# Kernel optimization log

Measured on AMD Instinct MI355X. Metric: run time of the kernel, lower is better.

## Reference

```python
import jax, jax.numpy as jnp
import numpy as np
from jax import lax

EPS = 1e-6


def setup_inputs() -> dict:
    key = jax.random.key(0)
    k1, k2, k3, k4 = jax.random.split(key, 4)
    B, M, N = 256, 256, 256
    A_re = jax.random.normal(k1, (B, M, N), dtype=jnp.float32)
    A_im = jax.random.normal(k2, (B, M, N), dtype=jnp.float32)
    v_re = jax.random.uniform(k3, (B, N, 1), dtype=jnp.float32)
    v_im = jax.random.uniform(k4, (B, N, 1), dtype=jnp.float32)
    return {"A_re": A_re, "A_im": A_im, "v_re": v_re, "v_im": v_im, "num_iter": 30}


def reference(A_re, A_im, v_re, v_im, num_iter):
    A = (A_re + 1j * A_im).astype(jnp.complex64)          # [B, M, N]
    v = (v_re + 1j * v_im).astype(jnp.complex64)          # [B, N, 1]
    # AhA = A^H A : [B, N, N]
    AhA = jnp.einsum('bmn,bmk->bnk', jnp.conj(A), A)

    def step(v, _):
        v = jnp.matmul(AhA, v)                            # [B, N, 1]
        # ||v||_2 over the N axis -> [B, 1]
        eig = jnp.sqrt(jnp.sum(v.real**2 + v.imag**2, axis=1))
        v = v / (eig[:, :, None] + EPS)
        return v, eig

    v, eigs = lax.scan(step, v, None, length=num_iter)
    return eigs[-1].reshape(-1)                           # [B]
```

## Files before the change

### kernel.cpp

```cpp
#include <hip/hip_runtime.h>
#include <cstdint>

typedef _Float16 f16;
typedef _Float16 f16x2 __attribute__((ext_vector_type(2)));
typedef _Float16 f16x8 __attribute__((ext_vector_type(8)));
typedef float    f32x4 __attribute__((ext_vector_type(4)));

static __device__ __forceinline__ uint32_t pack2(float x, float y) {
    f16 hx = (f16)x, hy = (f16)y;
    uint32_t ux = __builtin_bit_cast(unsigned short, hx);
    uint32_t uy = __builtin_bit_cast(unsigned short, hy);
    return ux | (uy << 16);
}

__global__ __launch_bounds__(512, 2) void k_gemm(const float* __restrict__ Are,
                                                 const float* __restrict__ Aim,
                                                 f16* __restrict__ AhAre,
                                                 f16* __restrict__ AhAim) {
    const int tid = threadIdx.x;
    const int b = blockIdx.x;

    __shared__ __align__(16) f16 ls[2][256 * 32];

    const int l = tid & 63, g = tid >> 6;
    const int lr = l & 15, lk = l >> 4;

    const int u = tid & 15;
    const int fp = tid >> 4;
    const int su = u >> 2, uq = u & 3;

    f32x4 cR[16], cI[16], dR[8], dI[8];
#pragma unroll
    for (int j = 0; j < 16; ++j) { cR[j] = (f32x4)0.0f; cI[j] = (f32x4)0.0f; }
#pragma unroll
    for (int j = 0; j < 8; ++j)  { dR[j] = (f32x4)0.0f; dI[j] = (f32x4)0.0f; }

    for (int m0 = 0; m0 < 256; m0 += 32) {
        __syncthreads();
        float4 v[2][4];
#pragma unroll
        for (int t = 0; t < 2; ++t) {
            const float* sp = (t ? Aim : Are) + (size_t)b * 65536
                            + (size_t)(m0 + 2 * u) * 256 + fp * 8;
            v[t][0] = *(const float4*)(sp);
            v[t][1] = *(const float4*)(sp + 4);
            v[t][2] = *(const float4*)(sp + 256);
            v[t][3] = *(const float4*)(sp + 260);
        }
#pragma unroll
        for (int t = 0; t < 2; ++t) {
            float xv[8] = {v[t][0].x, v[t][0].y, v[t][0].z, v[t][0].w,
                           v[t][1].x, v[t][1].y, v[t][1].z, v[t][1].w};
            float yv[8] = {v[t][2].x, v[t][2].y, v[t][2].z, v[t][2].w,
                           v[t][3].x, v[t][3].y, v[t][3].z, v[t][3].w};
            uint32_t* lw = (uint32_t*)&ls[t][0];
#pragma unroll
            for (int i = 0; i < 8; ++i) {
                int r = fp * 8 + i;
                int s = su ^ ((r >> 1) & 3);
                lw[r * 16 + s * 4 + uq] = pack2(xv[i], yv[i]);
            }
        }
        __syncthreads();

        const int r1 = 16 * g + lr;
        const int r2 = 128 + 16 * g + lr;
        const int s1 = lk ^ ((r1 >> 1) & 3);
        const int s2 = lk ^ ((r2 >> 1) & 3);
        f16x8 a1re = *(const f16x8*)(&ls[0][r1 * 32 + s1 * 8]);
        uint4 u1   = *(const uint4*)(&ls[1][r1 * 32 + s1 * 8]);
        f16x8 a2re = *(const f16x8*)(&ls[0][r2 * 32 + s2 * 8]);
        uint4 u2   = *(const uint4*)(&ls[1][r2 * 32 + s2 * 8]);
        f16x8 a1im = __builtin_bit_cast(f16x8, u1);
        f16x8 a2im = __builtin_bit_cast(f16x8, u2);
        uint4 n1 = make_uint4(u1.x ^ 0x80008000u, u1.y ^ 0x80008000u,
                              u1.z ^ 0x80008000u, u1.w ^ 0x80008000u);
        uint4 n2 = make_uint4(u2.x ^ 0x80008000u, u2.y ^ 0x80008000u,
                              u2.z ^ 0x80008000u, u2.w ^ 0x80008000u);
        f16x8 na1 = __builtin_bit_cast(f16x8, n1);
        f16x8 na2 = __builtin_bit_cast(f16x8, n2);

#pragma unroll
        for (int j = 0; j < 16; ++j) {
            int rb = 16 * j + lr;
            int sb = lk ^ ((rb >> 1) & 3);
            f16x8 bre = *(const f16x8*)(&ls[0][rb * 32 + sb * 8]);
            f16x8 bim = *(const f16x8*)(&ls[1][rb * 32 + sb * 8]);
            cR[j] = __builtin_amdgcn_mfma_f32_16x16x32_f16(a1re, bre, cR[j], 0, 0, 0);
            cR[j] = __builtin_amdgcn_mfma_f32_16x16x32_f16(a1im, bim, cR[j], 0, 0, 0);
            cI[j] = __builtin_amdgcn_mfma_f32_16x16x32_f16(a1re, bim, cI[j], 0, 0, 0);
            cI[j] = __builtin_amdgcn_mfma_f32_16x16x32_f16(na1,  bre, cI[j], 0, 0, 0);
            if (j >= 8) {
                dR[j-8] = __builtin_amdgcn_mfma_f32_16x16x32_f16(a2re, bre, dR[j-8], 0, 0, 0);
                dR[j-8] = __builtin_amdgcn_mfma_f32_16x16x32_f16(a2im, bim, dR[j-8], 0, 0, 0);
                dI[j-8] = __builtin_amdgcn_mfma_f32_16x16x32_f16(a2re, bim, dI[j-8], 0, 0, 0);
                dI[j-8] = __builtin_amdgcn_mfma_f32_16x16x32_f16(na2,  bre, dI[j-8], 0, 0, 0);
            }
        }
    }

    f16* oR = AhAre + (size_t)b * 65536;
    f16* oI = AhAim + (size_t)b * 65536;

#pragma unroll
    for (int j = 0; j < 16; ++j)
#pragma unroll
        for (int r = 0; r < 4; ++r) {
            int n = 16 * g + lk * 4 + r;
            int c = 16 * j + lr;
            oR[(size_t)n * 256 + c] = (f16)cR[j][r];
            oI[(size_t)n * 256 + c] = (f16)cI[j][r];
        }
#pragma unroll
    for (int j = 0; j < 8; ++j)
#pragma unroll
        for (int r = 0; r < 4; ++r) {
            int n = 128 + 16 * g + lk * 4 + r;
            int c = 128 + 16 * j + lr;
            oR[(size_t)n * 256 + c] = (f16)dR[j][r];
            oI[(size_t)n * 256 + c] = (f16)dI[j][r];
        }

    f16* lsm = &ls[0][0];
    const int jj_out = tid >> 2, qtr = tid & 3;

    __syncthreads();
#pragma unroll
    for (int j = 8; j < 16; ++j)
#pragma unroll
        for (int r = 0; r < 4; ++r) {
            int jj = 16 * (j - 8) + lr;
            int nn = 16 * g + lk * 4 + r;
            lsm[jj * 128 + nn] = (f16)cR[j][r];
        }
    __syncthreads();
    {
        const f16* srow = lsm + jj_out * 128 + qtr * 32;
        f16* drow = oR + (size_t)(128 + jj_out) * 256 + qtr * 32;
#pragma unroll
        for (int ch = 0; ch < 4; ++ch)
            *(uint4*)(void*)(drow + ch * 8) = *(const uint4*)(srow + ch * 8);
    }
    __syncthreads();
#pragma unroll
    for (int j = 8; j < 16; ++j)
#pragma unroll
        for (int r = 0; r < 4; ++r) {
            int jj = 16 * (j - 8) + lr;
            int nn = 16 * g + lk * 4 + r;
            lsm[jj * 128 + nn] = (f16)(-cI[j][r]);
        }
    __syncthreads();
    {
        const f16* srow = lsm + jj_out * 128 + qtr * 32;
        f16* drow = oI + (size_t)(128 + jj_out) * 256 + qtr * 32;
#pragma unroll
        for (int ch = 0; ch < 4; ++ch)
            *(uint4*)(void*)(drow + ch * 8) = *(const uint4*)(srow + ch * 8);
    }
}

static __device__ __forceinline__ void matvec2(const f16x8 (&afr)[2][16],
                                               const f16* __restrict__ vs, int h,
                                               float4 (&y)[2]) {
    f16x8 bf[16];
#pragma unroll
    for (int c = 0; c < 16; ++c) bf[c] = *(const f16x8*)(vs + 32 * c + 8 * h);
    f32x4 P0[2], P1[2];
#pragma unroll
    for (int rg = 0; rg < 2; ++rg) { P0[rg] = (f32x4)0.0f; P1[rg] = (f32x4)0.0f; }
#pragma unroll
    for (int c = 0; c < 16; ++c) {
#pragma unroll
        for (int rg = 0; rg < 2; ++rg) {
            if (c & 1) P1[rg] = __builtin_amdgcn_mfma_f32_16x16x32_f16(afr[rg][c], bf[c], P1[rg], 0, 0, 0);
            else       P0[rg] = __builtin_amdgcn_mfma_f32_16x16x32_f16(afr[rg][c], bf[c], P0[rg], 0, 0, 0);
        }
    }
#pragma unroll
    for (int rg = 0; rg < 2; ++rg)
        y[rg] = make_float4(P0[rg][0] + P1[rg][0], P0[rg][1] + P1[rg][1],
                            P0[rg][2] + P1[rg][2], P0[rg][3] + P1[rg][3]);
}

__global__ __launch_bounds__(512, 2) void k_power(const f16* __restrict__ AhAre,
                                                  const f16* __restrict__ AhAim,
                                                  const float* __restrict__ vre,
                                                  const float* __restrict__ vim,
                                                  const int* __restrict__ pniter,
                                                  float* __restrict__ out) {
    const int tid = threadIdx.x;
    const int b = blockIdx.x;
    const int l = tid & 63;
    const int g = tid >> 6;
    const int sel = l & 15;
    const int h = l >> 4;

    __shared__ __align__(16) f16 v0h[2][512];
    __shared__ __align__(16) f16 v1h[2][512];
    __shared__ __align__(16) float part[2][8];

    f16x8 afr[2][16];
#pragma unroll
    for (int rg = 0; rg < 2; ++rg) {
        const int m = 32 * g + 16 * rg + sel;
        const f16* bR = AhAre + (size_t)b * 65536 + (size_t)m * 256 + 8 * h;
        const f16* bI = AhAim + (size_t)b * 65536 + (size_t)m * 256 + 8 * h;
#pragma unroll
        for (int c = 0; c < 8; ++c) {
            afr[rg][c]     = *(const f16x8*)(bR + 32 * c);
            afr[rg][8 + c] = *(const f16x8*)(bI + 32 * c);
        }
    }
#pragma unroll
    for (int rg = 0; rg < 2; ++rg)
#pragma unroll
        for (int c = 0; c < 16; ++c) asm volatile("" : "+a"(afr[rg][c]));

    if (tid < 256) {
        float xr = vre[b * 256 + tid], xi = vim[b * 256 + tid];
        v0h[0][tid]       = (f16)xr;
        v0h[0][256 + tid] = (f16)(-xi);
        v1h[0][tid]       = (f16)xi;
        v1h[0][256 + tid] = (f16)xr;
    }
    __syncthreads();

    const int niter = *pniter;
    const f16* vsel = (sel == 0) ? &v0h[0][0] : &v1h[0][0];

    float eig = 0.0f;

    auto npart = [&](int wb, const float4 (&y)[2]) {
        float s_ = 0.0f;
        if (sel < 2) {
#pragma unroll
            for (int rg = 0; rg < 2; ++rg)
                s_ += y[rg].x * y[rg].x + y[rg].y * y[rg].y
                    + y[rg].z * y[rg].z + y[rg].w * y[rg].w;
        }
        s_ += __shfl_xor(s_, 1, 64);
        s_ += __shfl_xor(s_, 16, 64);
        s_ += __shfl_xor(s_, 32, 64);
        if (l == 0) part[wb][g] = s_;
    };
    auto vwrite = [&](int wb, const float4 (&y)[2], float sc) {
        if (sel < 2) {
#pragma unroll
            for (int rg = 0; rg < 2; ++rg) {
                uint32_t w0 = pack2(y[rg].x * sc, y[rg].y * sc);
                uint32_t w1 = pack2(y[rg].z * sc, y[rg].w * sc);
                int m0 = 32 * g + 16 * rg + 4 * h;
                if (sel == 0) {
                    *(uint2*)(void*)(&v0h[wb][m0])       = make_uint2(w0, w1);
                    *(uint2*)(void*)(&v1h[wb][256 + m0]) = make_uint2(w0, w1);
                } else {
                    *(uint2*)(void*)(&v1h[wb][m0])       = make_uint2(w0, w1);
                    *(uint2*)(void*)(&v0h[wb][256 + m0]) =
                        make_uint2(w0 ^ 0x80008000u, w1 ^ 0x80008000u);
                }
            }
        }
    };
    auto psum = [&](int rb) -> float {
        float4 q0 = *(const float4*)(&part[rb][0]);
        float4 q1 = *(const float4*)(&part[rb][4]);
        return (q0.x + q0.y + q0.z + q0.w) + (q1.x + q1.y + q1.z + q1.w);
    };

    float sc_m1 = 1.0f;
    float nm2   = 1.0f;

    float4 y[2];

    if (niter >= 1) {
        matvec2(afr, vsel, h, y);
        npart(1, y);
        __syncthreads();
        float e1v = sqrtf(psum(1));
        float sc  = __builtin_amdgcn_rcpf(e1v + 1e-6f);
        vwrite(1, y, sc);
        eig = e1v;
        __syncthreads();
    }
    if (niter >= 2) {
        matvec2(afr, vsel + 512, h, y);
        npart(0, y);
        __syncthreads();
        float e2v = sqrtf(psum(0));
        float sc  = __builtin_amdgcn_rcpf(e2v + 1e-6f);
        vwrite(0, y, sc);
        eig = e2v;
        sc_m1 = sc;
        nm2   = 1.0f;
        __syncthreads();
    }

    int wr = 0;
    for (int t = 3; t <= niter; ++t) {
        const int rd = wr;
        wr ^= 1;
        float q   = psum(rd);
        float e1v = __builtin_amdgcn_sqrtf(q);
        float nm1 = e1v * sc_m1;
        float sc  = nm2 * __builtin_amdgcn_rcpf(e1v * nm1 + 1e-12f);
        matvec2(afr, vsel + (size_t)rd * 512, h, y);
        vwrite(wr, y, sc);
        npart(wr, y);
        nm2 = nm1; sc_m1 = sc;
        __syncthreads();
    }

    if (niter >= 3) {
        float qT = psum(wr);
        eig = sqrtf(qT) / (nm2 + 1e-12f);
    }
    if (tid == 0) out[b] = eig;
}

extern "C" void kernel_launch(void* const* d_in, const int* in_sizes, int n_in,
                              void* d_out, int out_size, void* d_ws, size_t ws_size,
                              hipStream_t stream) {
    const float* Are = (const float*)d_in[0];
    const float* Aim = (const float*)d_in[1];
    const float* vre = (const float*)d_in[2];
    const float* vim = (const float*)d_in[3];
    const int* niter = (const int*)d_in[4];
    float* out = (float*)d_out;

    f16* AhAre = (f16*)d_ws;
    f16* AhAim = (f16*)((char*)d_ws + (size_t)32 * 1024 * 1024);

    k_gemm<<<dim3(256), dim3(512), 0, stream>>>(Are, Aim, AhAre, AhAim);
    k_power<<<dim3(256), dim3(512), 0, stream>>>(AhAre, AhAim, vre, vim, niter, out);
}
```

Before: 97.59 us.

## Double-buffer LDS and prefetch next A tile during MFMA compute

Allocates two LDS buffers for the A^H A gemm and loads the next 32-row slab of A into registers while the current slab is being consumed by MFMAs. This removes one barrier per step and overlaps global load latency with compute. It doubles the LDS footprint and keeps prefetch registers live across the MFMA loop, which may raise register pressure.

Result: slower. 115.9 us (+18.7%).

```diff
diff --git a/kernel.cpp b/kernel.cpp
--- a/kernel.cpp
+++ b/kernel.cpp
@@ -20,7 +20,7 @@
     const int tid = threadIdx.x;
     const int b = blockIdx.x;
 
-    __shared__ __align__(16) f16 ls[2][256 * 32];
+    __shared__ __align__(16) f16 ls[2][2][256 * 32];
 
     const int l = tid & 63, g = tid >> 6;
     const int lr = l & 15, lk = l >> 4;
@@ -35,25 +35,28 @@
 #pragma unroll
     for (int j = 0; j < 8; ++j)  { dR[j] = (f32x4)0.0f; dI[j] = (f32x4)0.0f; }
 
-    for (int m0 = 0; m0 < 256; m0 += 32) {
-        __syncthreads();
-        float4 v[2][4];
-#pragma unroll
-        for (int t = 0; t < 2; ++t) {
-            const float* sp = (t ? Aim : Are) + (size_t)b * 65536
-                            + (size_t)(m0 + 2 * u) * 256 + fp * 8;
-            v[t][0] = *(const float4*)(sp);
-            v[t][1] = *(const float4*)(sp + 4);
-            v[t][2] = *(const float4*)(sp + 256);
-            v[t][3] = *(const float4*)(sp + 260);
-        }
+    float4 v[2][4];
+#pragma unroll
+    for (int t = 0; t < 2; ++t) {
+        const float* sp = (t ? Aim : Are) + (size_t)b * 65536
+                        + (size_t)(2 * u) * 256 + fp * 8;
+        v[t][0] = *(const float4*)(sp);
+        v[t][1] = *(const float4*)(sp + 4);
+        v[t][2] = *(const float4*)(sp + 256);
+        v[t][3] = *(const float4*)(sp + 260);
+    }
+
+#pragma unroll 2
+    for (int step = 0; step < 8; ++step) {
+        const int p = step & 1;
+
 #pragma unroll
         for (int t = 0; t < 2; ++t) {
             float xv[8] = {v[t][0].x, v[t][0].y, v[t][0].z, v[t][0].w,
                            v[t][1].x, v[t][1].y, v[t][1].z, v[t][1].w};
             float yv[8] = {v[t][2].x, v[t][2].y, v[t][2].z, v[t][2].w,
                            v[t][3].x, v[t][3].y, v[t][3].z, v[t][3].w};
-            uint32_t* lw = (uint32_t*)&ls[t][0];
+            uint32_t* lw = (uint32_t*)&ls[p][t][0];
 #pragma unroll
             for (int i = 0; i < 8; ++i) {
                 int r = fp * 8 + i;
@@ -61,16 +64,33 @@
                 lw[r * 16 + s * 4 + uq] = pack2(xv[i], yv[i]);
             }
         }
-        __syncthreads();
+
+        if (step < 7) {
+            const int m0n = 32 * (step + 1);
+#pragma unroll
+            for (int t = 0; t < 2; ++t) {
+                const float* sp = (t ? Aim : Are) + (size_t)b * 65536
+                                + (size_t)(m0n + 2 * u) * 256 + fp * 8;
+                v[t][0] = *(const float4*)(sp);
+                v[t][1] = *(const float4*)(sp + 4);
+                v[t][2] = *(const float4*)(sp + 256);
+                v[t][3] = *(const float4*)(sp + 260);
+            }
+        }
+
+        __syncthreads();
+
+        const f16* lsR = &ls[p][0][0];
+        const f16* lsI = &ls[p][1][0];
 
         const int r1 = 16 * g + lr;
         const int r2 = 128 + 16 * g + lr;
         const int s1 = lk ^ ((r1 >> 1) & 3);
         const int s2 = lk ^ ((r2 >> 1) & 3);
-        f16x8 a1re = *(const f16x8*)(&ls[0][r1 * 32 + s1 * 8]);
-        uint4 u1   = *(const uint4*)(&ls[1][r1 * 32 + s1 * 8]);
-        f16x8 a2re = *(const f16x8*)(&ls[0][r2 * 32 + s2 * 8]);
-        uint4 u2   = *(const uint4*)(&ls[1][r2 * 32 + s2 * 8]);
+        f16x8 a1re = *(const f16x8*)(&lsR[r1 * 32 + s1 * 8]);
+        uint4 u1   = *(const uint4*)(&lsI[r1 * 32 + s1 * 8]);
+        f16x8 a2re = *(const f16x8*)(&lsR[r2 * 32 + s2 * 8]);
+        uint4 u2   = *(const uint4*)(&lsI[r2 * 32 + s2 * 8]);
         f16x8 a1im = __builtin_bit_cast(f16x8, u1);
         f16x8 a2im = __builtin_bit_cast(f16x8, u2);
         uint4 n1 = make_uint4(u1.x ^ 0x80008000u, u1.y ^ 0x80008000u,
@@ -84,8 +104,8 @@
         for (int j = 0; j < 16; ++j) {
             int rb = 16 * j + lr;
             int sb = lk ^ ((rb >> 1) & 3);
-            f16x8 bre = *(const f16x8*)(&ls[0][rb * 32 + sb * 8]);
-            f16x8 bim = *(const f16x8*)(&ls[1][rb * 32 + sb * 8]);
+            f16x8 bre = *(const f16x8*)(&lsR[rb * 32 + sb * 8]);
+            f16x8 bim = *(const f16x8*)(&lsI[rb * 32 + sb * 8]);
             cR[j] = __builtin_amdgcn_mfma_f32_16x16x32_f16(a1re, bre, cR[j], 0, 0, 0);
             cR[j] = __builtin_amdgcn_mfma_f32_16x16x32_f16(a1im, bim, cR[j], 0, 0, 0);
             cI[j] = __builtin_amdgcn_mfma_f32_16x16x32_f16(a1re, bim, cI[j], 0, 0, 0);
@@ -121,7 +141,7 @@
             oI[(size_t)n * 256 + c] = (f16)dI[j][r];
         }
 
-    f16* lsm = &ls[0][0];
+    f16* lsm = &ls[0][0][0];
     const int jj_out = tid >> 2, qtr = tid & 3;
 
     __syncthreads();
```

## Split Hermitian Gram GEMM into three quadrant blocks per batch

Applied to the files above, without the earlier changes.

The A^H A kernel now launches three blocks per batch, each computing one 128x128 quadrant of the Hermitian result (top-left, top-right with mirrored lower-left, bottom-right), instead of one block computing the whole upper triangle. Each block holds half as many accumulators, so launch bounds rise to allow four blocks per CU. A remapping of the block index groups the three blocks of the same batch so they land on the same XCD and share A in cache. This adds parallelism and occupancy on 256 CUs, at the cost of re-reading A from memory or cache up to three times per batch.

Result: slower. 117.0 us (+19.9%).

```diff
diff --git a/kernel.cpp b/kernel.cpp
--- a/kernel.cpp
+++ b/kernel.cpp
@@ -2,7 +2,6 @@
 #include <cstdint>
 
 typedef _Float16 f16;
-typedef _Float16 f16x2 __attribute__((ext_vector_type(2)));
 typedef _Float16 f16x8 __attribute__((ext_vector_type(8)));
 typedef float    f32x4 __attribute__((ext_vector_type(4)));
 
@@ -13,76 +12,84 @@
     return ux | (uy << 16);
 }
 
-__global__ __launch_bounds__(512, 2) void k_gemm(const float* __restrict__ Are,
+__global__ __launch_bounds__(512, 4) void k_gemm(const float* __restrict__ Are,
                                                  const float* __restrict__ Aim,
                                                  f16* __restrict__ AhAre,
                                                  f16* __restrict__ AhAim) {
     const int tid = threadIdx.x;
-    const int b = blockIdx.x;
+    int bid0 = blockIdx.x;
+    int bid = (bid0 & 7) * 96 + (bid0 >> 3);
+    const int b  = bid / 3;
+    const int qq = bid - 3 * b;
+    const int R0 = (qq == 2) ? 128 : 0;
+    const int C0 = (qq == 0) ? 0 : 128;
+    const int nb0 = (qq == 2) ? 128 : 0;
+    const int boff = (qq == 1) ? 128 : 0;
 
     __shared__ __align__(16) f16 ls[2][256 * 32];
 
     const int l = tid & 63, g = tid >> 6;
     const int lr = l & 15, lk = l >> 4;
-
-    const int u = tid & 15;
-    const int fp = tid >> 4;
+    const int u = tid & 15, fp = tid >> 4;
     const int su = u >> 2, uq = u & 3;
 
-    f32x4 cR[16], cI[16], dR[8], dI[8];
-#pragma unroll
-    for (int j = 0; j < 16; ++j) { cR[j] = (f32x4)0.0f; cI[j] = (f32x4)0.0f; }
-#pragma unroll
-    for (int j = 0; j < 8; ++j)  { dR[j] = (f32x4)0.0f; dI[j] = (f32x4)0.0f; }
+    f16* oR = AhAre + (size_t)b * 65536;
+    f16* oI = AhAim + (size_t)b * 65536;
+
+    f32x4 cR[8], cI[8];
+#pragma unroll
+    for (int j = 0; j < 8; ++j) { cR[j] = (f32x4)0.0f; cI[j] = (f32x4)0.0f; }
 
     for (int m0 = 0; m0 < 256; m0 += 32) {
         __syncthreads();
-        float4 v[2][4];
 #pragma unroll
         for (int t = 0; t < 2; ++t) {
             const float* sp = (t ? Aim : Are) + (size_t)b * 65536
-                            + (size_t)(m0 + 2 * u) * 256 + fp * 8;
-            v[t][0] = *(const float4*)(sp);
-            v[t][1] = *(const float4*)(sp + 4);
-            v[t][2] = *(const float4*)(sp + 256);
-            v[t][3] = *(const float4*)(sp + 260);
-        }
-#pragma unroll
-        for (int t = 0; t < 2; ++t) {
-            float xv[8] = {v[t][0].x, v[t][0].y, v[t][0].z, v[t][0].w,
-                           v[t][1].x, v[t][1].y, v[t][1].z, v[t][1].w};
-            float yv[8] = {v[t][2].x, v[t][2].y, v[t][2].z, v[t][2].w,
-                           v[t][3].x, v[t][3].y, v[t][3].z, v[t][3].w};
+                            + (size_t)(m0 + 2 * u) * 256 + nb0 + fp * 4;
+            float4 x = *(const float4*)(sp);
+            float4 y = *(const float4*)(sp + 256);
+            float xv[4] = {x.x, x.y, x.z, x.w};
+            float yv[4] = {y.x, y.y, y.z, y.w};
             uint32_t* lw = (uint32_t*)&ls[t][0];
 #pragma unroll
-            for (int i = 0; i < 8; ++i) {
-                int r = fp * 8 + i;
+            for (int i = 0; i < 4; ++i) {
+                int r = fp * 4 + i;
                 int s = su ^ ((r >> 1) & 3);
                 lw[r * 16 + s * 4 + uq] = pack2(xv[i], yv[i]);
             }
         }
-        __syncthreads();
-
-        const int r1 = 16 * g + lr;
-        const int r2 = 128 + 16 * g + lr;
-        const int s1 = lk ^ ((r1 >> 1) & 3);
-        const int s2 = lk ^ ((r2 >> 1) & 3);
-        f16x8 a1re = *(const f16x8*)(&ls[0][r1 * 32 + s1 * 8]);
-        uint4 u1   = *(const uint4*)(&ls[1][r1 * 32 + s1 * 8]);
-        f16x8 a2re = *(const f16x8*)(&ls[0][r2 * 32 + s2 * 8]);
-        uint4 u2   = *(const uint4*)(&ls[1][r2 * 32 + s2 * 8]);
+        if (qq == 1) {
+#pragma unroll
+            for (int t = 0; t < 2; ++t) {
+                const float* sp = (t ? Aim : Are) + (size_t)b * 65536
+                                + (size_t)(m0 + 2 * u) * 256 + 128 + fp * 4;
+                float4 x = *(const float4*)(sp);
+                float4 y = *(const float4*)(sp + 256);
+                float xv[4] = {x.x, x.y, x.z, x.w};
+                float yv[4] = {y.x, y.y, y.z, y.w};
+                uint32_t* lw = (uint32_t*)&ls[t][0];
+#pragma unroll
+                for (int i = 0; i < 4; ++i) {
+                    int r = 128 + fp * 4 + i;
+                    int s = su ^ ((r >> 1) & 3);
+                    lw[r * 16 + s * 4 + uq] = pack2(xv[i], yv[i]);
+                }
+            }
+        }
+        __syncthreads();
+
+        const int ra = 16 * g + lr;
+        const int sa = lk ^ ((ra >> 1) & 3);
+        f16x8 a1re = *(const f16x8*)(&ls[0][ra * 32 + sa * 8]);
+        uint4 u1   = *(const uint4*)(&ls[1][ra * 32 + sa * 8]);
         f16x8 a1im = __builtin_bit_cast(f16x8, u1);
-        f16x8 a2im = __builtin_bit_cast(f16x8, u2);
         uint4 n1 = make_uint4(u1.x ^ 0x80008000u, u1.y ^ 0x80008000u,
                               u1.z ^ 0x80008000u, u1.w ^ 0x80008000u);
-        uint4 n2 = make_uint4(u2.x ^ 0x80008000u, u2.y ^ 0x80008000u,
-                              u2.z ^ 0x80008000u, u2.w ^ 0x80008000u);
         f16x8 na1 = __builtin_bit_cast(f16x8, n1);
-        f16x8 na2 = __builtin_bit_cast(f16x8, n2);
-
-#pragma unroll
-        for (int j = 0; j < 16; ++j) {
-            int rb = 16 * j + lr;
+
+#pragma unroll
+        for (int j = 0; j < 8; ++j) {
+            int rb = boff + 16 * j + lr;
             int sb = lk ^ ((rb >> 1) & 3);
             f16x8 bre = *(const f16x8*)(&ls[0][rb * 32 + sb * 8]);
             f16x8 bim = *(const f16x8*)(&ls[1][rb * 32 + sb * 8]);
@@ -90,73 +97,57 @@
             cR[j] = __builtin_amdgcn_mfma_f32_16x16x32_f16(a1im, bim, cR[j], 0, 0, 0);
             cI[j] = __builtin_amdgcn_mfma_f32_16x16x32_f16(a1re, bim, cI[j], 0, 0, 0);
             cI[j] = __builtin_amdgcn_mfma_f32_16x16x32_f16(na1,  bre, cI[j], 0, 0, 0);
-            if (j >= 8) {
-                dR[j-8] = __builtin_amdgcn_mfma_f32_16x16x32_f16(a2re, bre, dR[j-8], 0, 0, 0);
-                dR[j-8] = __builtin_amdgcn_mfma_f32_16x16x32_f16(a2im, bim, dR[j-8], 0, 0, 0);
-                dI[j-8] = __builtin_amdgcn_mfma_f32_16x16x32_f16(a2re, bim, dI[j-8], 0, 0, 0);
-                dI[j-8] = __builtin_amdgcn_mfma_f32_16x16x32_f16(na2,  bre, dI[j-8], 0, 0, 0);
-            }
-        }
-    }
-
-    f16* oR = AhAre + (size_t)b * 65536;
-    f16* oI = AhAim + (size_t)b * 65536;
-
-#pragma unroll
-    for (int j = 0; j < 16; ++j)
+        }
+    }
+
+#pragma unroll
+    for (int j = 0; j < 8; ++j)
 #pragma unroll
         for (int r = 0; r < 4; ++r) {
-            int n = 16 * g + lk * 4 + r;
-            int c = 16 * j + lr;
+            int n = R0 + 16 * g + lk * 4 + r;
+            int c = C0 + 16 * j + lr;
             oR[(size_t)n * 256 + c] = (f16)cR[j][r];
             oI[(size_t)n * 256 + c] = (f16)cI[j][r];
         }
-#pragma unroll
-    for (int j = 0; j < 8; ++j)
-#pragma unroll
-        for (int r = 0; r < 4; ++r) {
-            int n = 128 + 16 * g + lk * 4 + r;
-            int c = 128 + 16 * j + lr;
-            oR[(size_t)n * 256 + c] = (f16)dR[j][r];
-            oI[(size_t)n * 256 + c] = (f16)dI[j][r];
-        }
-
-    f16* lsm = &ls[0][0];
-    const int jj_out = tid >> 2, qtr = tid & 3;
-
-    __syncthreads();
-#pragma unroll
-    for (int j = 8; j < 16; ++j)
-#pragma unroll
-        for (int r = 0; r < 4; ++r) {
-            int jj = 16 * (j - 8) + lr;
-            int nn = 16 * g + lk * 4 + r;
-            lsm[jj * 128 + nn] = (f16)cR[j][r];
-        }
-    __syncthreads();
-    {
-        const f16* srow = lsm + jj_out * 128 + qtr * 32;
-        f16* drow = oR + (size_t)(128 + jj_out) * 256 + qtr * 32;
-#pragma unroll
-        for (int ch = 0; ch < 4; ++ch)
-            *(uint4*)(void*)(drow + ch * 8) = *(const uint4*)(srow + ch * 8);
-    }
-    __syncthreads();
-#pragma unroll
-    for (int j = 8; j < 16; ++j)
-#pragma unroll
-        for (int r = 0; r < 4; ++r) {
-            int jj = 16 * (j - 8) + lr;
-            int nn = 16 * g + lk * 4 + r;
-            lsm[jj * 128 + nn] = (f16)(-cI[j][r]);
-        }
-    __syncthreads();
-    {
-        const f16* srow = lsm + jj_out * 128 + qtr * 32;
-        f16* drow = oI + (size_t)(128 + jj_out) * 256 + qtr * 32;
-#pragma unroll
-        for (int ch = 0; ch < 4; ++ch)
-            *(uint4*)(void*)(drow + ch * 8) = *(const uint4*)(srow + ch * 8);
+
+    if (qq == 1) {
+        f16* lsm = &ls[0][0];
+        const int jjo = tid >> 2, qtr = tid & 3;
+
+        __syncthreads();
+#pragma unroll
+        for (int j = 0; j < 8; ++j)
+#pragma unroll
+            for (int r = 0; r < 4; ++r) {
+                int jj = 16 * j + lr;
+                int nn = 16 * g + lk * 4 + r;
+                lsm[jj * 128 + nn] = (f16)cR[j][r];
+            }
+        __syncthreads();
+        {
+            const f16* srow = lsm + jjo * 128 + qtr * 32;
+            f16* drow = oR + (size_t)(128 + jjo) * 256 + qtr * 32;
+#pragma unroll
+            for (int ch = 0; ch < 4; ++ch)
+                *(uint4*)(void*)(drow + ch * 8) = *(const uint4*)(srow + ch * 8);
+        }
+        __syncthreads();
+#pragma unroll
+        for (int j = 0; j < 8; ++j)
+#pragma unroll
+            for (int r = 0; r < 4; ++r) {
+                int jj = 16 * j + lr;
+                int nn = 16 * g + lk * 4 + r;
+                lsm[jj * 128 + nn] = (f16)(-cI[j][r]);
+            }
+        __syncthreads();
+        {
+            const f16* srow = lsm + jjo * 128 + qtr * 32;
+            f16* drow = oI + (size_t)(128 + jjo) * 256 + qtr * 32;
+#pragma unroll
+            for (int ch = 0; ch < 4; ++ch)
+                *(uint4*)(void*)(drow + ch * 8) = *(const uint4*)(srow + ch * 8);
+        }
     }
 }
 
@@ -331,6 +322,6 @@
     f16* AhAre = (f16*)d_ws;
     f16* AhAim = (f16*)((char*)d_ws + (size_t)32 * 1024 * 1024);
 
-    k_gemm<<<dim3(256), dim3(512), 0, stream>>>(Are, Aim, AhAre, AhAim);
+    k_gemm<<<dim3(768), dim3(512), 0, stream>>>(Are, Aim, AhAre, AhAim);
     k_power<<<dim3(256), dim3(512), 0, stream>>>(AhAre, AhAim, vre, vim, niter, out);
 }
```

## Split Hermitian GEMM into two phases with 64-deep K tiles and prefetch

Applied to the files above, without the earlier changes.

Restructures the A^H A kernel into two sequential phases: the first computes the top 128 rows (16 accumulator tiles), the second computes only the bottom-right block and loads just the right half of the columns. Each phase stages 64 rows of M per iteration and prefetches the next global tile into registers while the MFMAs run. Custom barriers with waitcnt and sched_barrier replace __syncthreads. This aims to shorten accumulator live ranges, hide global-load latency and halve barrier count, at the cost of doubled LDS footprint, which may reduce occupancy, and of re-reading A for the second phase.

After: 107.1 us. 9.8% more time.

```diff
diff --git a/kernel.cpp b/kernel.cpp
--- a/kernel.cpp
+++ b/kernel.cpp
@@ -2,7 +2,6 @@
 #include <cstdint>
 
 typedef _Float16 f16;
-typedef _Float16 f16x2 __attribute__((ext_vector_type(2)));
 typedef _Float16 f16x8 __attribute__((ext_vector_type(8)));
 typedef float    f32x4 __attribute__((ext_vector_type(4)));
 
@@ -11,6 +10,13 @@
     uint32_t ux = __builtin_bit_cast(unsigned short, hx);
     uint32_t uy = __builtin_bit_cast(unsigned short, hy);
     return ux | (uy << 16);
+}
+
+static __device__ __forceinline__ void lds_barrier() {
+    __builtin_amdgcn_sched_barrier(0);
+    asm volatile("s_waitcnt lgkmcnt(0)");
+    __builtin_amdgcn_s_barrier();
+    __builtin_amdgcn_sched_barrier(0);
 }
 
 __global__ __launch_bounds__(512, 2) void k_gemm(const float* __restrict__ Are,
@@ -20,143 +26,215 @@
     const int tid = threadIdx.x;
     const int b = blockIdx.x;
 
-    __shared__ __align__(16) f16 ls[2][256 * 32];
+    __shared__ __align__(16) f16 ls[2][256 * 64];
 
     const int l = tid & 63, g = tid >> 6;
     const int lr = l & 15, lk = l >> 4;
-
-    const int u = tid & 15;
-    const int fp = tid >> 4;
+    const int u = tid & 15, fp = tid >> 4;
     const int su = u >> 2, uq = u & 3;
-
-    f32x4 cR[16], cI[16], dR[8], dI[8];
-#pragma unroll
-    for (int j = 0; j < 16; ++j) { cR[j] = (f32x4)0.0f; cI[j] = (f32x4)0.0f; }
-#pragma unroll
-    for (int j = 0; j < 8; ++j)  { dR[j] = (f32x4)0.0f; dI[j] = (f32x4)0.0f; }
-
-    for (int m0 = 0; m0 < 256; m0 += 32) {
-        __syncthreads();
-        float4 v[2][4];
-#pragma unroll
-        for (int t = 0; t < 2; ++t) {
-            const float* sp = (t ? Aim : Are) + (size_t)b * 65536
-                            + (size_t)(m0 + 2 * u) * 256 + fp * 8;
-            v[t][0] = *(const float4*)(sp);
-            v[t][1] = *(const float4*)(sp + 4);
-            v[t][2] = *(const float4*)(sp + 256);
-            v[t][3] = *(const float4*)(sp + 260);
-        }
-#pragma unroll
-        for (int t = 0; t < 2; ++t) {
-            float xv[8] = {v[t][0].x, v[t][0].y, v[t][0].z, v[t][0].w,
-                           v[t][1].x, v[t][1].y, v[t][1].z, v[t][1].w};
-            float yv[8] = {v[t][2].x, v[t][2].y, v[t][2].z, v[t][2].w,
-                           v[t][3].x, v[t][3].y, v[t][3].z, v[t][3].w};
-            uint32_t* lw = (uint32_t*)&ls[t][0];
-#pragma unroll
-            for (int i = 0; i < 8; ++i) {
-                int r = fp * 8 + i;
-                int s = su ^ ((r >> 1) & 3);
-                lw[r * 16 + s * 4 + uq] = pack2(xv[i], yv[i]);
-            }
-        }
-        __syncthreads();
-
-        const int r1 = 16 * g + lr;
-        const int r2 = 128 + 16 * g + lr;
-        const int s1 = lk ^ ((r1 >> 1) & 3);
-        const int s2 = lk ^ ((r2 >> 1) & 3);
-        f16x8 a1re = *(const f16x8*)(&ls[0][r1 * 32 + s1 * 8]);
-        uint4 u1   = *(const uint4*)(&ls[1][r1 * 32 + s1 * 8]);
-        f16x8 a2re = *(const f16x8*)(&ls[0][r2 * 32 + s2 * 8]);
-        uint4 u2   = *(const uint4*)(&ls[1][r2 * 32 + s2 * 8]);
-        f16x8 a1im = __builtin_bit_cast(f16x8, u1);
-        f16x8 a2im = __builtin_bit_cast(f16x8, u2);
-        uint4 n1 = make_uint4(u1.x ^ 0x80008000u, u1.y ^ 0x80008000u,
-                              u1.z ^ 0x80008000u, u1.w ^ 0x80008000u);
-        uint4 n2 = make_uint4(u2.x ^ 0x80008000u, u2.y ^ 0x80008000u,
-                              u2.z ^ 0x80008000u, u2.w ^ 0x80008000u);
-        f16x8 na1 = __builtin_bit_cast(f16x8, n1);
-        f16x8 na2 = __builtin_bit_cast(f16x8, n2);
-
-#pragma unroll
-        for (int j = 0; j < 16; ++j) {
-            int rb = 16 * j + lr;
-            int sb = lk ^ ((rb >> 1) & 3);
-            f16x8 bre = *(const f16x8*)(&ls[0][rb * 32 + sb * 8]);
-            f16x8 bim = *(const f16x8*)(&ls[1][rb * 32 + sb * 8]);
-            cR[j] = __builtin_amdgcn_mfma_f32_16x16x32_f16(a1re, bre, cR[j], 0, 0, 0);
-            cR[j] = __builtin_amdgcn_mfma_f32_16x16x32_f16(a1im, bim, cR[j], 0, 0, 0);
-            cI[j] = __builtin_amdgcn_mfma_f32_16x16x32_f16(a1re, bim, cI[j], 0, 0, 0);
-            cI[j] = __builtin_amdgcn_mfma_f32_16x16x32_f16(na1,  bre, cI[j], 0, 0, 0);
-            if (j >= 8) {
-                dR[j-8] = __builtin_amdgcn_mfma_f32_16x16x32_f16(a2re, bre, dR[j-8], 0, 0, 0);
-                dR[j-8] = __builtin_amdgcn_mfma_f32_16x16x32_f16(a2im, bim, dR[j-8], 0, 0, 0);
-                dI[j-8] = __builtin_amdgcn_mfma_f32_16x16x32_f16(a2re, bim, dI[j-8], 0, 0, 0);
-                dI[j-8] = __builtin_amdgcn_mfma_f32_16x16x32_f16(na2,  bre, dI[j-8], 0, 0, 0);
-            }
-        }
-    }
 
     f16* oR = AhAre + (size_t)b * 65536;
     f16* oI = AhAim + (size_t)b * 65536;
 
-#pragma unroll
-    for (int j = 0; j < 16; ++j)
-#pragma unroll
-        for (int r = 0; r < 4; ++r) {
-            int n = 16 * g + lk * 4 + r;
-            int c = 16 * j + lr;
-            oR[(size_t)n * 256 + c] = (f16)cR[j][r];
-            oI[(size_t)n * 256 + c] = (f16)cI[j][r];
-        }
-#pragma unroll
-    for (int j = 0; j < 8; ++j)
-#pragma unroll
-        for (int r = 0; r < 4; ++r) {
-            int n = 128 + 16 * g + lk * 4 + r;
-            int c = 128 + 16 * j + lr;
-            oR[(size_t)n * 256 + c] = (f16)dR[j][r];
-            oI[(size_t)n * 256 + c] = (f16)dI[j][r];
-        }
-
-    f16* lsm = &ls[0][0];
-    const int jj_out = tid >> 2, qtr = tid & 3;
-
-    __syncthreads();
-#pragma unroll
-    for (int j = 8; j < 16; ++j)
-#pragma unroll
-        for (int r = 0; r < 4; ++r) {
-            int jj = 16 * (j - 8) + lr;
-            int nn = 16 * g + lk * 4 + r;
-            lsm[jj * 128 + nn] = (f16)cR[j][r];
-        }
-    __syncthreads();
     {
-        const f16* srow = lsm + jj_out * 128 + qtr * 32;
-        f16* drow = oR + (size_t)(128 + jj_out) * 256 + qtr * 32;
-#pragma unroll
-        for (int ch = 0; ch < 4; ++ch)
-            *(uint4*)(void*)(drow + ch * 8) = *(const uint4*)(srow + ch * 8);
-    }
-    __syncthreads();
-#pragma unroll
-    for (int j = 8; j < 16; ++j)
-#pragma unroll
-        for (int r = 0; r < 4; ++r) {
-            int jj = 16 * (j - 8) + lr;
-            int nn = 16 * g + lk * 4 + r;
-            lsm[jj * 128 + nn] = (f16)(-cI[j][r]);
-        }
-    __syncthreads();
+        f32x4 cR[16], cI[16];
+#pragma unroll
+        for (int j = 0; j < 16; ++j) { cR[j] = (f32x4)0.0f; cI[j] = (f32x4)0.0f; }
+
+        float4 v[2][2][4];
+        auto load0 = [&](int m0) {
+#pragma unroll
+            for (int t = 0; t < 2; ++t)
+#pragma unroll
+                for (int sub = 0; sub < 2; ++sub) {
+                    const float* sp = (t ? Aim : Are) + (size_t)b * 65536
+                                    + (size_t)(m0 + 32 * sub + 2 * u) * 256 + fp * 8;
+                    v[t][sub][0] = *(const float4*)(sp);
+                    v[t][sub][1] = *(const float4*)(sp + 4);
+                    v[t][sub][2] = *(const float4*)(sp + 256);
+                    v[t][sub][3] = *(const float4*)(sp + 260);
+                }
+        };
+
+        load0(0);
+
+#pragma unroll
+        for (int step = 0; step < 4; ++step) {
+#pragma unroll
+            for (int t = 0; t < 2; ++t)
+#pragma unroll
+                for (int sub = 0; sub < 2; ++sub) {
+                    float xv[8] = {v[t][sub][0].x, v[t][sub][0].y, v[t][sub][0].z, v[t][sub][0].w,
+                                   v[t][sub][1].x, v[t][sub][1].y, v[t][sub][1].z, v[t][sub][1].w};
+                    float yv[8] = {v[t][sub][2].x, v[t][sub][2].y, v[t][sub][2].z, v[t][sub][2].w,
+                                   v[t][sub][3].x, v[t][sub][3].y, v[t][sub][3].z, v[t][sub][3].w};
+                    uint32_t* lw = (uint32_t*)&ls[t][0];
+#pragma unroll
+                    for (int i = 0; i < 8; ++i) {
+                        int r = fp * 8 + i;
+                        int s = su ^ ((r >> 1) & 3);
+                        lw[r * 32 + sub * 16 + s * 4 + uq] = pack2(xv[i], yv[i]);
+                    }
+                }
+
+            lds_barrier();
+
+            if (step < 3) load0(64 * (step + 1));
+            __builtin_amdgcn_sched_barrier(0);
+
+#pragma unroll
+            for (int sub = 0; sub < 2; ++sub) {
+                const int ra = 16 * g + lr;
+                const int sa = lk ^ ((ra >> 1) & 3);
+                f16x8 are = *(const f16x8*)(&ls[0][ra * 64 + sub * 32 + sa * 8]);
+                uint4 u1  = *(const uint4*)(&ls[1][ra * 64 + sub * 32 + sa * 8]);
+                f16x8 aim = __builtin_bit_cast(f16x8, u1);
+                uint4 n1 = make_uint4(u1.x ^ 0x80008000u, u1.y ^ 0x80008000u,
+                                      u1.z ^ 0x80008000u, u1.w ^ 0x80008000u);
+                f16x8 nai = __builtin_bit_cast(f16x8, n1);
+#pragma unroll
+                for (int j = 0; j < 16; ++j) {
+                    int rb = 16 * j + lr;
+                    int sb = lk ^ ((rb >> 1) & 3);
+                    f16x8 bre = *(const f16x8*)(&ls[0][rb * 64 + sub * 32 + sb * 8]);
+                    f16x8 bim = *(const f16x8*)(&ls[1][rb * 64 + sub * 32 + sb * 8]);
+                    cR[j] = __builtin_amdgcn_mfma_f32_16x16x32_f16(are, bre, cR[j], 0, 0, 0);
+                    cR[j] = __builtin_amdgcn_mfma_f32_16x16x32_f16(aim, bim, cR[j], 0, 0, 0);
+                    cI[j] = __builtin_amdgcn_mfma_f32_16x16x32_f16(are, bim, cI[j], 0, 0, 0);
+                    cI[j] = __builtin_amdgcn_mfma_f32_16x16x32_f16(nai, bre, cI[j], 0, 0, 0);
+                }
+            }
+
+            lds_barrier();
+        }
+
+#pragma unroll
+        for (int j = 0; j < 16; ++j)
+#pragma unroll
+            for (int r = 0; r < 4; ++r) {
+                int n = 16 * g + lk * 4 + r;
+                int c = 16 * j + lr;
+                oR[(size_t)n * 256 + c] = (f16)cR[j][r];
+                oI[(size_t)n * 256 + c] = (f16)cI[j][r];
+            }
+
+        f16* lsm = &ls[0][0];
+        const int jj_out = tid >> 2, qtr = tid & 3;
+
+        __syncthreads();
+#pragma unroll
+        for (int j = 8; j < 16; ++j)
+#pragma unroll
+            for (int r = 0; r < 4; ++r) {
+                int jj = 16 * (j - 8) + lr;
+                int nn = 16 * g + lk * 4 + r;
+                lsm[jj * 128 + nn] = (f16)cR[j][r];
+            }
+        __syncthreads();
+        {
+            const f16* srow = lsm + jj_out * 128 + qtr * 32;
+            f16* drow = oR + (size_t)(128 + jj_out) * 256 + qtr * 32;
+#pragma unroll
+            for (int ch = 0; ch < 4; ++ch)
+                *(uint4*)(void*)(drow + ch * 8) = *(const uint4*)(srow + ch * 8);
+        }
+        __syncthreads();
+#pragma unroll
+        for (int j = 8; j < 16; ++j)
+#pragma unroll
+            for (int r = 0; r < 4; ++r) {
+                int jj = 16 * (j - 8) + lr;
+                int nn = 16 * g + lk * 4 + r;
+                lsm[jj * 128 + nn] = (f16)(-cI[j][r]);
+            }
+        __syncthreads();
+        {
+            const f16* srow = lsm + jj_out * 128 + qtr * 32;
+            f16* drow = oI + (size_t)(128 + jj_out) * 256 + qtr * 32;
+#pragma unroll
+            for (int ch = 0; ch < 4; ++ch)
+                *(uint4*)(void*)(drow + ch * 8) = *(const uint4*)(srow + ch * 8);
+        }
+        __syncthreads();
+    }
+
     {
-        const f16* srow = lsm + jj_out * 128 + qtr * 32;
-        f16* drow = oI + (size_t)(128 + jj_out) * 256 + qtr * 32;
-#pragma unroll
-        for (int ch = 0; ch < 4; ++ch)
-            *(uint4*)(void*)(drow + ch * 8) = *(const uint4*)(srow + ch * 8);
+        f32x4 dR[8], dI[8];
+#pragma unroll
+        for (int j = 0; j < 8; ++j) { dR[j] = (f32x4)0.0f; dI[j] = (f32x4)0.0f; }
+
+        float4 w[2][2][2];
+        auto load1 = [&](int m0) {
+#pragma unroll
+            for (int t = 0; t < 2; ++t)
+#pragma unroll
+                for (int sub = 0; sub < 2; ++sub) {
+                    const float* sp = (t ? Aim : Are) + (size_t)b * 65536
+                                    + (size_t)(m0 + 32 * sub + 2 * u) * 256 + 128 + fp * 4;
+                    w[t][sub][0] = *(const float4*)(sp);
+                    w[t][sub][1] = *(const float4*)(sp + 256);
+                }
+        };
+
+        load1(0);
+
+#pragma unroll
+        for (int step = 0; step < 4; ++step) {
+#pragma unroll
+            for (int t = 0; t < 2; ++t)
+#pragma unroll
+                for (int sub = 0; sub < 2; ++sub) {
+                    float xv[4] = {w[t][sub][0].x, w[t][sub][0].y, w[t][sub][0].z, w[t][sub][0].w};
+                    float yv[4] = {w[t][sub][1].x, w[t][sub][1].y, w[t][sub][1].z, w[t][sub][1].w};
+                    uint32_t* lw = (uint32_t*)&ls[t][0];
+#pragma unroll
+                    for (int i = 0; i < 4; ++i) {
+                        int r = fp * 4 + i;
+                        int s = su ^ ((r >> 1) & 3);
+                        lw[r * 32 + sub * 16 + s * 4 + uq] = pack2(xv[i], yv[i]);
+                    }
+                }
+
+            lds_barrier();
+
+            if (step < 3) load1(64 * (step + 1));
+            __builtin_amdgcn_sched_barrier(0);
+
+#pragma unroll
+            for (int sub = 0; sub < 2; ++sub) {
+                const int ra = 16 * g + lr;
+                const int sa = lk ^ ((ra >> 1) & 3);
+                f16x8 are = *(const f16x8*)(&ls[0][ra * 64 + sub * 32 + sa * 8]);
+                uint4 u2  = *(const uint4*)(&ls[1][ra * 64 + sub * 32 + sa * 8]);
+                f16x8 aim = __builtin_bit_cast(f16x8, u2);
+                uint4 n2 = make_uint4(u2.x ^ 0x80008000u, u2.y ^ 0x80008000u,
+                                      u2.z ^ 0x80008000u, u2.w ^ 0x80008000u);
+                f16x8 nai = __builtin_bit_cast(f16x8, n2);
+#pragma unroll
+                for (int j = 0; j < 8; ++j) {
+                    int rb = 16 * j + lr;
+                    int sb = lk ^ ((rb >> 1) & 3);
+                    f16x8 bre = *(const f16x8*)(&ls[0][rb * 64 + sub * 32 + sb * 8]);
+                    f16x8 bim = *(const f16x8*)(&ls[1][rb * 64 + sub * 32 + sb * 8]);
+                    dR[j] = __builtin_amdgcn_mfma_f32_16x16x32_f16(are, bre, dR[j], 0, 0, 0);
+                    dR[j] = __builtin_amdgcn_mfma_f32_16x16x32_f16(aim, bim, dR[j], 0, 0, 0);
+                    dI[j] = __builtin_amdgcn_mfma_f32_16x16x32_f16(are, bim, dI[j], 0, 0, 0);
+                    dI[j] = __builtin_amdgcn_mfma_f32_16x16x32_f16(nai, bre, dI[j], 0, 0, 0);
+                }
+            }
+
+            lds_barrier();
+        }
+
+#pragma unroll
+        for (int j = 0; j < 8; ++j)
+#pragma unroll
+            for (int r = 0; r < 4; ++r) {
+                int n = 128 + 16 * g + lk * 4 + r;
+                int c = 128 + 16 * j + lr;
+                oR[(size_t)n * 256 + c] = (f16)dR[j][r];
+                oI[(size_t)n * 256 + c] = (f16)dI[j][r];
+            }
     }
 }
 
```
